# Optimization experiments

Hardware: AMD Instinct MI355X
Metric: run time of the kernel (lower is better)

Reference implementation:

```python
import jax, jax.numpy as jnp
import numpy as np


def setup_inputs() -> dict:
    key = jax.random.key(0)
    ks = jax.random.split(key, 6)
    B, N, D_in, D, Dg, H = 32, 256, 512, 256, 256, 512
    s = lambda f_in: 1.0 / np.sqrt(f_in)
    return {
        "xi": jax.random.normal(ks[0], (B, N, D_in), dtype=jnp.float32),
        "W_img": jax.random.normal(ks[1], (D_in, D), dtype=jnp.float32) * s(D_in),
        "b_img": jnp.zeros((D,), jnp.float32),
        "W_gnn_self": jax.random.normal(ks[2], (D, Dg), dtype=jnp.float32) * s(D),
        "W_gnn_nbr": jax.random.normal(ks[3], (D, Dg), dtype=jnp.float32) * s(D),
        "b_gnn": jnp.zeros((Dg,), jnp.float32),
        "W1": jax.random.normal(ks[4], (N * Dg, H), dtype=jnp.float32) * s(N * Dg),
        "b1": jnp.zeros((H,), jnp.float32),
        "W2": jax.random.normal(ks[5], (H, 1), dtype=jnp.float32) * s(H),
        "b2": jnp.zeros((1,), jnp.float32),
        "k": 10,
    }


def _knn_edges(xie, k):
    # xie: [B, N, D]. Per-image squared euclidean cdist + top-k (exclude self).
    B, N, _ = xie.shape
    x2 = jnp.sum(xie * xie, axis=-1)  # [B, N]
    d2 = x2[:, :, None] + x2[:, None, :] - 2.0 * jnp.einsum("bnd,bmd->bnm", xie, xie)
    big = jnp.asarray(1e30, d2.dtype)
    d2 = d2 + big * jnp.eye(N, dtype=d2.dtype)  # exclude self
    _, nbr = jax.lax.top_k(-d2, k)  # [B, N, k] neighbor (source) indices
    tgt = jnp.broadcast_to(jnp.arange(N)[None, :, None], (B, N, k))
    return nbr, tgt


def reference(xi, W_img, b_img, W_gnn_self, W_gnn_nbr, b_gnn, W1, b1, W2, b2, k):
    B, N, _ = xi.shape
    # image encoder -> per-node embeddings [B, N, D]
    xie = xi @ W_img + b_img
    # KNN graph build per image, then shift indices into one batched graph
    nbr, tgt = _knn_edges(xie, k)
    shift = (jnp.arange(B) * N)[:, None, None]
    src = (nbr + shift).reshape(-1)  # [B*N*k]
    dst = (tgt + shift).reshape(-1)  # [B*N*k]
    # batched graph conv: mean neighbor aggregation + self transform
    x_flat = xie.reshape(B * N, -1)
    agg = jax.ops.segment_sum(x_flat[src], dst, num_segments=B * N) / k
    gep = jax.nn.relu(x_flat @ W_gnn_self + agg @ W_gnn_nbr + b_gnn)
    gep = gep.reshape(B, N, -1)  # split_batch_graph
    # estimation MLP on flattened graph embedding
    h = jax.nn.relu(gep.reshape(B, -1) @ W1 + b1)
    out = h @ W2 + b2  # [B, 1]
    return xie, gep, out
```

## Files before the change

### kernel.cpp

```cpp
#include <hip/hip_runtime.h>

#define BB 32
#define NN 256
#define DIN 512
#define DD 256
#define HH 512
#define MM 8192
#define NDG 65536
#define KSTR 16

typedef __attribute__((ext_vector_type(8))) __bf16 bf16x8;
typedef __attribute__((ext_vector_type(4))) float f32x4;
typedef unsigned short ushort_t;

__device__ __forceinline__ unsigned short f2bf(float x) {
  unsigned u = __float_as_uint(x);
  u += 0x7FFFu + ((u >> 16) & 1u);
  return (unsigned short)(u >> 16);
}

__global__ __launch_bounds__(512) void k_enc(const float* __restrict__ A,
                                             const float* __restrict__ W,
                                             const float* __restrict__ bias,
                                             float* __restrict__ C,
                                             ushort_t* __restrict__ A_bf) {
  __shared__ float Asm[32][520];
  const int tid = threadIdx.x;
  const int mb0 = blockIdx.x * 32;
  const int cg = tid & 31;
  const int mh = (tid >> 5) & 7;
  const int team = tid >> 8;
#pragma unroll
  for (int i = 0; i < 8; ++i) {
    int idx = tid + i * 512;
    int m = idx >> 7;
    int kq = idx & 127;
    float4 v = *reinterpret_cast<const float4*>(&A[(size_t)(mb0 + m) * DIN + kq * 4]);
    *reinterpret_cast<float4*>(&Asm[m][kq * 4]) = v;
  }
  __syncthreads();
  float4 acc[4][2] = {};
  const int kt0 = team * 256;
  const float* wp = &W[(size_t)kt0 * DD + cg * 8];
  float4 wA[4][2], wB[4][2];
#pragma unroll
  for (int j = 0; j < 4; ++j) {
    wA[j][0] = *reinterpret_cast<const float4*>(&wp[(size_t)j * DD]);
    wA[j][1] = *reinterpret_cast<const float4*>(&wp[(size_t)j * DD + 4]);
  }
  for (int it = 0; it < 64; ++it) {
    if (it < 63) {
#pragma unroll
      for (int j = 0; j < 4; ++j) {
        wB[j][0] = *reinterpret_cast<const float4*>(&wp[(size_t)((it + 1) * 4 + j) * DD]);
        wB[j][1] = *reinterpret_cast<const float4*>(&wp[(size_t)((it + 1) * 4 + j) * DD + 4]);
      }
    }
    const int kk = kt0 + it * 4;
#pragma unroll
    for (int r = 0; r < 4; ++r) {
      float4 a = *reinterpret_cast<const float4*>(&Asm[mh * 4 + r][kk]);
#pragma unroll
      for (int h = 0; h < 2; ++h) {
        acc[r][h].x += a.x * wA[0][h].x; acc[r][h].y += a.x * wA[0][h].y;
        acc[r][h].z += a.x * wA[0][h].z; acc[r][h].w += a.x * wA[0][h].w;
        acc[r][h].x += a.y * wA[1][h].x; acc[r][h].y += a.y * wA[1][h].y;
        acc[r][h].z += a.y * wA[1][h].z; acc[r][h].w += a.y * wA[1][h].w;
        acc[r][h].x += a.z * wA[2][h].x; acc[r][h].y += a.z * wA[2][h].y;
        acc[r][h].z += a.z * wA[2][h].z; acc[r][h].w += a.z * wA[2][h].w;
        acc[r][h].x += a.w * wA[3][h].x; acc[r][h].y += a.w * wA[3][h].y;
        acc[r][h].z += a.w * wA[3][h].z; acc[r][h].w += a.w * wA[3][h].w;
      }
    }
#pragma unroll
    for (int j = 0; j < 4; ++j) {
      wA[j][0] = wB[j][0]; wA[j][1] = wB[j][1];
    }
  }
  __syncthreads();
  float* red = &Asm[0][0];
  if (team == 1) {
#pragma unroll
    for (int r = 0; r < 4; ++r) {
      *reinterpret_cast<float4*>(&red[(mh * 4 + r) * 256 + cg * 8]) = acc[r][0];
      *reinterpret_cast<float4*>(&red[(mh * 4 + r) * 256 + cg * 8 + 4]) = acc[r][1];
    }
  }
  __syncthreads();
  if (team == 0) {
    float4 bv0 = *reinterpret_cast<const float4*>(&bias[cg * 8]);
    float4 bv1 = *reinterpret_cast<const float4*>(&bias[cg * 8 + 4]);
#pragma unroll
    for (int r = 0; r < 4; ++r) {
      const int row = mb0 + mh * 4 + r;
      float4 o0 = *reinterpret_cast<float4*>(&red[(mh * 4 + r) * 256 + cg * 8]);
      float4 o1 = *reinterpret_cast<float4*>(&red[(mh * 4 + r) * 256 + cg * 8 + 4]);
      float4 s0, s1;
      s0.x = acc[r][0].x + o0.x + bv0.x; s0.y = acc[r][0].y + o0.y + bv0.y;
      s0.z = acc[r][0].z + o0.z + bv0.z; s0.w = acc[r][0].w + o0.w + bv0.w;
      s1.x = acc[r][1].x + o1.x + bv1.x; s1.y = acc[r][1].y + o1.y + bv1.y;
      s1.z = acc[r][1].z + o1.z + bv1.z; s1.w = acc[r][1].w + o1.w + bv1.w;
      *reinterpret_cast<float4*>(&C[(size_t)row * DD + cg * 8]) = s0;
      *reinterpret_cast<float4*>(&C[(size_t)row * DD + cg * 8 + 4]) = s1;
      ushort4 ob0, ob1;
      ob0.x = f2bf(s0.x); ob0.y = f2bf(s0.y); ob0.z = f2bf(s0.z); ob0.w = f2bf(s0.w);
      ob1.x = f2bf(s1.x); ob1.y = f2bf(s1.y); ob1.z = f2bf(s1.z); ob1.w = f2bf(s1.w);
      *reinterpret_cast<ushort4*>(&A_bf[(size_t)row * 512 + cg * 8]) = ob0;
      *reinterpret_cast<ushort4*>(&A_bf[(size_t)row * 512 + cg * 8 + 4]) = ob1;
    }
  }
}

__global__ __launch_bounds__(256) void k_norm(const float* __restrict__ X,
                                              float* __restrict__ x2) {
  const int tid = threadIdx.x;
  const int row = blockIdx.x * 4 + (tid >> 6);
  const int lane = tid & 63;
  float4 v = *reinterpret_cast<const float4*>(&X[(size_t)row * DD + lane * 4]);
  float s = v.x * v.x + v.y * v.y + v.z * v.z + v.w * v.w;
#pragma unroll
  for (int off = 1; off < 64; off <<= 1) s += __shfl_xor(s, off);
  if (lane == 0) x2[row] = s;
}

__global__ __launch_bounds__(256) void k_dist(const float* __restrict__ X,
                                              const float* __restrict__ x2,
                                              float* __restrict__ d2) {
  __shared__ float As[16][68];
  __shared__ float Bs[16][68];
  const int tid = threadIdx.x;
  const int b = blockIdx.z;
  const int m0 = blockIdx.x * 64, n0 = blockIdx.y * 64;
  const float* Xb = X + b * NN * DD;
  const int tx = tid & 15, ty = tid >> 4;
  const int lrow = tid >> 2, lfc = (tid & 3) * 4;
  float acc[4][4] = {};
  for (int k0 = 0; k0 < DD; k0 += 16) {
    float4 va = *reinterpret_cast<const float4*>(&Xb[(n0 + lrow) * DD + k0 + lfc]);
    As[lfc + 0][lrow] = va.x; As[lfc + 1][lrow] = va.y;
    As[lfc + 2][lrow] = va.z; As[lfc + 3][lrow] = va.w;
    float4 vb = *reinterpret_cast<const float4*>(&Xb[(m0 + lrow) * DD + k0 + lfc]);
    Bs[lfc + 0][lrow] = vb.x; Bs[lfc + 1][lrow] = vb.y;
    Bs[lfc + 2][lrow] = vb.z; Bs[lfc + 3][lrow] = vb.w;
    __syncthreads();
#pragma unroll
    for (int kk = 0; kk < 16; ++kk) {
      float a[4], bv[4];
      *reinterpret_cast<float4*>(a) = *reinterpret_cast<float4*>(&As[kk][ty * 4]);
      *reinterpret_cast<float4*>(bv) = *reinterpret_cast<float4*>(&Bs[kk][tx * 4]);
#pragma unroll
      for (int i = 0; i < 4; ++i)
#pragma unroll
        for (int j = 0; j < 4; ++j) acc[i][j] += a[i] * bv[j];
    }
    __syncthreads();
  }
#pragma unroll
  for (int i = 0; i < 4; ++i) {
    const int n = n0 + ty * 4 + i;
    const float xn = x2[b * NN + n];
    float4 v;
    float* vv = reinterpret_cast<float*>(&v);
#pragma unroll
    for (int j = 0; j < 4; ++j) {
      const int mc = m0 + tx * 4 + j;
      float dv = xn + x2[b * NN + mc] - 2.0f * acc[i][j];
      if (n == mc) dv = 1e30f;
      vv[j] = dv;
    }
    *reinterpret_cast<float4*>(&d2[(size_t)(b * NN + n) * NN + m0 + tx * 4]) = v;
  }
}

__global__ __launch_bounds__(256) void k_topk(const float* __restrict__ d2,
                                              const int* __restrict__ kp,
                                              int* __restrict__ nbr) {
  const int tid = threadIdx.x;
  const int i = blockIdx.x * 4 + (tid >> 6);
  const int lane = tid & 63;
  const int kcnt = kp[0];
  const float* row = d2 + (size_t)i * NN;
  float v0 = row[lane];
  float v1 = row[lane + 64];
  float v2 = row[lane + 128];
  float v3 = row[lane + 192];
  for (int it = 0; it < kcnt; ++it) {
    float v = v0; int idx = lane;
    if (v1 < v) { v = v1; idx = lane + 64; }
    if (v2 < v) { v = v2; idx = lane + 128; }
    if (v3 < v) { v = v3; idx = lane + 192; }
#pragma unroll
    for (int off = 1; off < 64; off <<= 1) {
      float ov = __shfl_xor(v, off);
      int oi = __shfl_xor(idx, off);
      if (ov < v || (ov == v && oi < idx)) { v = ov; idx = oi; }
    }
    if (lane == 0) nbr[i * KSTR + it] = idx;
    const int slot = idx >> 6;
    if (lane == (idx & 63)) {
      if (slot == 0) v0 = 3e38f;
      else if (slot == 1) v1 = 3e38f;
      else if (slot == 2) v2 = 3e38f;
      else v3 = 3e38f;
    }
  }
}

__global__ __launch_bounds__(256) void k_agg(const float* __restrict__ X,
                                             const int* __restrict__ nbr,
                                             const int* __restrict__ kp,
                                             ushort_t* __restrict__ A_bf) {
  const int i = blockIdx.x;
  const int b = i >> 8;
  const int t = threadIdx.x;
  const int kcnt = kp[0];
  float acc = 0.0f;
  for (int j = 0; j < kcnt; ++j) {
    const int nb = nbr[i * KSTR + j];
    acc += X[(size_t)(b * NN + nb) * DD + t];
  }
  A_bf[(size_t)i * 512 + 256 + t] = f2bf(acc / (float)kcnt);
}

__global__ __launch_bounds__(256) void k_cvtw(const float* __restrict__ Ws,
                                              const float* __restrict__ Wn,
                                              ushort_t* __restrict__ B_bfT) {
  const int id = blockIdx.x * 256 + threadIdx.x;
  const int k = id >> 8;
  const int n = id & 255;
  float v = (k < 256) ? Ws[(size_t)k * 256 + n] : Wn[(size_t)(k - 256) * 256 + n];
  B_bfT[(size_t)n * 512 + k] = f2bf(v);
}

__global__ __launch_bounds__(256) void k_gnn(const ushort_t* __restrict__ A_bf,
                                             const ushort_t* __restrict__ B_bfT,
                                             const float* __restrict__ bias,
                                             float* __restrict__ C,
                                             ushort_t* __restrict__ gep_bf) {
  __shared__ ushort_t As[64 * 72];
  __shared__ ushort_t Bs[64 * 72];
  const int tid = threadIdx.x;
  const int m0 = blockIdx.x * 64, n0 = blockIdx.y * 64;
  const int l = tid & 63, w = tid >> 6;
  const int mw = (w & 1) * 32, nw = (w >> 1) * 32;
  const int lr = tid >> 3, lq = tid & 7;
  f32x4 acc[2][2] = {};
  for (int kt = 0; kt < 8; ++kt) {
    const int kb = kt * 64;
#pragma unroll
    for (int s = 0; s < 2; ++s) {
      const int r = lr + s * 32;
      uint4 va = *reinterpret_cast<const uint4*>(&A_bf[(size_t)(m0 + r) * 512 + kb + lq * 8]);
      *reinterpret_cast<uint4*>(&As[r * 72 + lq * 8]) = va;
      uint4 vb = *reinterpret_cast<const uint4*>(&B_bfT[(size_t)(n0 + r) * 512 + kb + lq * 8]);
      *reinterpret_cast<uint4*>(&Bs[r * 72 + lq * 8]) = vb;
    }
    __syncthreads();
#pragma unroll
    for (int ks = 0; ks < 2; ++ks) {
      bf16x8 af[2], bf[2];
#pragma unroll
      for (int mi = 0; mi < 2; ++mi)
        af[mi] = *reinterpret_cast<const bf16x8*>(
            &As[(mw + mi * 16 + (l & 15)) * 72 + ks * 32 + (l >> 4) * 8]);
#pragma unroll
      for (int ni = 0; ni < 2; ++ni)
        bf[ni] = *reinterpret_cast<const bf16x8*>(
            &Bs[(nw + ni * 16 + (l & 15)) * 72 + ks * 32 + (l >> 4) * 8]);
#pragma unroll
      for (int mi = 0; mi < 2; ++mi)
#pragma unroll
        for (int ni = 0; ni < 2; ++ni)
          acc[mi][ni] = __builtin_amdgcn_mfma_f32_16x16x32_bf16(af[mi], bf[ni],
                                                                acc[mi][ni], 0, 0, 0);
    }
    __syncthreads();
  }
#pragma unroll
  for (int mi = 0; mi < 2; ++mi) {
    const int row_base = m0 + mw + mi * 16 + (l >> 4) * 4;
#pragma unroll
    for (int ni = 0; ni < 2; ++ni) {
      const int col = n0 + nw + ni * 16 + (l & 15);
      const float bv = bias[col];
#pragma unroll
      for (int r = 0; r < 4; ++r) {
        float v = acc[mi][ni][r] + bv;
        v = v > 0.0f ? v : 0.0f;
        C[(size_t)(row_base + r) * 256 + col] = v;
        gep_bf[(size_t)(row_base + r) * 256 + col] = f2bf(v);
      }
    }
  }
}

typedef const float __attribute__((address_space(1)))* gas1f;
typedef unsigned int __attribute__((address_space(3)))* las3u;

__global__ __launch_bounds__(256) void k_mlp1(const ushort_t* __restrict__ gep_bf,
                                              const float* __restrict__ W1,
                                              float* __restrict__ part) {
  __shared__ float Wb[2][32 * 512];
  __shared__ ushort_t Ab[32][264];
  const int tid = threadIdx.x;
  const int b = blockIdx.x;
  const int l = tid & 63, w = tid >> 6;
#pragma unroll
  for (int i = 0; i < 4; ++i) {
    int id = tid + i * 256;
    int m = id >> 5, dq8 = (id & 31) * 8;
    *reinterpret_cast<uint4*>(&Ab[m][dq8]) = *reinterpret_cast<const uint4*>(
        &gep_bf[((size_t)m * 256 + b) * 256 + dq8]);
  }
  const float* Wbase = W1 + (size_t)b * 256 * 512;
  auto stage = [&](int kt, int buf) {
    const float* gsrc = Wbase + (size_t)kt * 32 * 512;
#pragma unroll
    for (int i = 0; i < 16; ++i) {
      const int idx = w * 16 + i;
      const float* gp = gsrc + idx * 256 + l * 4;
      __builtin_amdgcn_global_load_lds((gas1f)gp, (las3u)&Wb[buf][idx * 256], 16, 0, 0);
    }
  };
  stage(0, 0);
  __syncthreads();
  const int n0w = w * 128;
  f32x4 acc[2][8] = {};
  for (int kt = 0; kt < 8; ++kt) {
    const int cur = kt & 1;
    if (kt < 7) stage(kt + 1, cur ^ 1);
    bf16x8 a[2];
#pragma unroll
    for (int mi = 0; mi < 2; ++mi)
      a[mi] = *reinterpret_cast<const bf16x8*>(&Ab[mi * 16 + (l & 15)][kt * 32 + (l >> 4) * 8]);
    const float* wl = &Wb[cur][0];
    const int kr = (l >> 4) * 8;
#pragma unroll
    for (int nf = 0; nf < 8; ++nf) {
      const int col = n0w + nf * 16 + (l & 15);
      union { unsigned short us[8]; bf16x8 v; } bb;
#pragma unroll
      for (int j = 0; j < 8; ++j)
        bb.us[j] = f2bf(wl[(kr + j) * 512 + col]);
      acc[0][nf] = __builtin_amdgcn_mfma_f32_16x16x32_bf16(a[0], bb.v, acc[0][nf], 0, 0, 0);
      acc[1][nf] = __builtin_amdgcn_mfma_f32_16x16x32_bf16(a[1], bb.v, acc[1][nf], 0, 0, 0);
    }
    __syncthreads();
  }
#pragma unroll
  for (int mi = 0; mi < 2; ++mi)
#pragma unroll
    for (int nf = 0; nf < 8; ++nf) {
      const int col = n0w + nf * 16 + (l & 15);
#pragma unroll
      for (int r = 0; r < 4; ++r) {
        const int m = mi * 16 + (l >> 4) * 4 + r;
        part[((size_t)b * 32 + m) * HH + col] = acc[mi][nf][r];
      }
    }
}

__global__ __launch_bounds__(256) void k_mlp1r(const float* __restrict__ part,
                                               const float* __restrict__ b1,
                                               float* __restrict__ h) {
  __shared__ float red[3][64];
  const int tid = threadIdx.x;
  const int m = blockIdx.x >> 3;
  const int c = (blockIdx.x & 7) * 64 + (tid & 63);
  const int bq = tid >> 6;
  float s = 0.0f;
  for (int bb = bq * 64; bb < bq * 64 + 64; ++bb)
    s += part[((size_t)bb * 32 + m) * 512 + c];
  if (bq > 0) red[bq - 1][tid & 63] = s;
  __syncthreads();
  if (bq == 0) {
    s += red[0][tid & 63] + red[1][tid & 63] + red[2][tid & 63];
    s += b1[c];
    h[m * HH + c] = s > 0.0f ? s : 0.0f;
  }
}

__global__ __launch_bounds__(256) void k_out(const float* __restrict__ h,
                                             const float* __restrict__ W2,
                                             const float* __restrict__ b2,
                                             float* __restrict__ outp) {
  const int tid = threadIdx.x;
  const int m = blockIdx.x * 4 + (tid >> 6);
  const int lane = tid & 63;
  float s = 0.0f;
#pragma unroll
  for (int j = 0; j < 8; ++j) s += h[m * HH + lane + 64 * j] * W2[lane + 64 * j];
#pragma unroll
  for (int off = 1; off < 64; off <<= 1) s += __shfl_xor(s, off);
  if (lane == 0) outp[m] = s + b2[0];
}

extern "C" void kernel_launch(void* const* d_in, const int* in_sizes, int n_in,
                              void* d_out, int out_size, void* d_ws, size_t ws_size,
                              hipStream_t stream) {
  const float* xi     = (const float*)d_in[0];
  const float* W_img  = (const float*)d_in[1];
  const float* b_img  = (const float*)d_in[2];
  const float* W_self = (const float*)d_in[3];
  const float* W_nbr  = (const float*)d_in[4];
  const float* b_gnn  = (const float*)d_in[5];
  const float* W1     = (const float*)d_in[6];
  const float* b1     = (const float*)d_in[7];
  const float* W2     = (const float*)d_in[8];
  const float* b2     = (const float*)d_in[9];
  const int*   kp     = (const int*)d_in[10];

  float* xie  = (float*)d_out;
  float* gep  = xie + (size_t)MM * DD;
  float* outp = gep + (size_t)MM * DD;

  float* ws   = (float*)d_ws;
  float* x2   = ws;
  int*   nbr  = (int*)(ws + 8192);
  float* d2   = ws + 8192 + 131072;
  float* part = d2 + (size_t)2097152;
  float* hbuf = part + (size_t)4194304;
  ushort_t* A_bf   = (ushort_t*)(hbuf + 16384);
  ushort_t* B_bfT  = A_bf + (size_t)MM * 512;
  ushort_t* gep_bf = B_bfT + 131072;

  k_enc  <<<MM / 32, 512, 0, stream>>>(xi, W_img, b_img, xie, A_bf);
  k_cvtw <<<512, 256, 0, stream>>>(W_self, W_nbr, B_bfT);
  k_norm <<<MM / 4, 256, 0, stream>>>(xie, x2);
  k_dist <<<dim3(4, 4, BB), 256, 0, stream>>>(xie, x2, d2);
  k_topk <<<MM / 4, 256, 0, stream>>>(d2, kp, nbr);
  k_agg  <<<MM, 256, 0, stream>>>(xie, nbr, kp, A_bf);
  k_gnn  <<<dim3(128, 4), 256, 0, stream>>>(A_bf, B_bfT, b_gnn, gep, gep_bf);
  k_mlp1 <<<256, 256, 0, stream>>>(gep_bf, W1, part);
  k_mlp1r<<<256, 256, 0, stream>>>(part, b1, hbuf);
  k_out  <<<8, 256, 0, stream>>>(hbuf, W2, b2, outp);
}
```

Measured before the change: 160.0 us.

## Fuse distance, top-k and aggregation into one kernel; merge MLP tail kernels

The encoder now also writes a transposed copy of the embeddings, so the new fused kernel can compute each 32-row distance block against the whole image. Top-k selection and neighbor mean aggregation then run in the same kernel, which removes the d2 and nbr round trips through global memory and two launches. The final reduction, ReLU and output dot product are merged into a single kernel. In exchange there are fewer blocks (256) for the distance work, an extra transposed write in the encoder, and the final kernel's 32 blocks each read the full partial buffer serially.

Result: slower. 230.6 us (+44.1%).

```diff
diff --git a/kernel.cpp b/kernel.cpp
--- a/kernel.cpp
+++ b/kernel.cpp
@@ -6,7 +6,6 @@
 #define DD 256
 #define HH 512
 #define MM 8192
-#define NDG 65536
 #define KSTR 16
 
 typedef __attribute__((ext_vector_type(8))) __bf16 bf16x8;
@@ -23,7 +22,8 @@
                                              const float* __restrict__ W,
                                              const float* __restrict__ bias,
                                              float* __restrict__ C,
-                                             ushort_t* __restrict__ A_bf) {
+                                             ushort_t* __restrict__ A_bf,
+                                             float* __restrict__ xieT) {
   __shared__ float Asm[32][520];
   const int tid = threadIdx.x;
   const int mb0 = blockIdx.x * 32;
@@ -107,7 +107,23 @@
       ob1.x = f2bf(s1.x); ob1.y = f2bf(s1.y); ob1.z = f2bf(s1.z); ob1.w = f2bf(s1.w);
       *reinterpret_cast<ushort4*>(&A_bf[(size_t)row * 512 + cg * 8]) = ob0;
       *reinterpret_cast<ushort4*>(&A_bf[(size_t)row * 512 + cg * 8 + 4]) = ob1;
-    }
+      *reinterpret_cast<float4*>(&red[(mh * 4 + r) * 256 + cg * 8]) = s0;
+      *reinterpret_cast<float4*>(&red[(mh * 4 + r) * 256 + cg * 8 + 4]) = s1;
+    }
+  }
+  __syncthreads();
+  {
+    const int b = mb0 >> 8;
+    const int n0b = mb0 & 255;
+    const int d = tid >> 1;
+    const int nh = (tid & 1) * 16;
+    float tmp[16];
+#pragma unroll
+    for (int i = 0; i < 16; ++i) tmp[i] = red[(nh + i) * 256 + d];
+    float* dst = &xieT[((size_t)b * 256 + d) * 256 + n0b + nh];
+#pragma unroll
+    for (int i = 0; i < 4; ++i)
+      *reinterpret_cast<float4*>(&dst[i * 4]) = *reinterpret_cast<float4*>(&tmp[i * 4]);
   }
 }
 
@@ -123,103 +139,112 @@
   if (lane == 0) x2[row] = s;
 }
 
-__global__ __launch_bounds__(256) void k_dist(const float* __restrict__ X,
-                                              const float* __restrict__ x2,
-                                              float* __restrict__ d2) {
-  __shared__ float As[16][68];
-  __shared__ float Bs[16][68];
-  const int tid = threadIdx.x;
-  const int b = blockIdx.z;
-  const int m0 = blockIdx.x * 64, n0 = blockIdx.y * 64;
-  const float* Xb = X + b * NN * DD;
-  const int tx = tid & 15, ty = tid >> 4;
-  const int lrow = tid >> 2, lfc = (tid & 3) * 4;
-  float acc[4][4] = {};
-  for (int k0 = 0; k0 < DD; k0 += 16) {
-    float4 va = *reinterpret_cast<const float4*>(&Xb[(n0 + lrow) * DD + k0 + lfc]);
-    As[lfc + 0][lrow] = va.x; As[lfc + 1][lrow] = va.y;
-    As[lfc + 2][lrow] = va.z; As[lfc + 3][lrow] = va.w;
-    float4 vb = *reinterpret_cast<const float4*>(&Xb[(m0 + lrow) * DD + k0 + lfc]);
-    Bs[lfc + 0][lrow] = vb.x; Bs[lfc + 1][lrow] = vb.y;
-    Bs[lfc + 2][lrow] = vb.z; Bs[lfc + 3][lrow] = vb.w;
-    __syncthreads();
-#pragma unroll
-    for (int kk = 0; kk < 16; ++kk) {
-      float a[4], bv[4];
-      *reinterpret_cast<float4*>(a) = *reinterpret_cast<float4*>(&As[kk][ty * 4]);
-      *reinterpret_cast<float4*>(bv) = *reinterpret_cast<float4*>(&Bs[kk][tx * 4]);
-#pragma unroll
-      for (int i = 0; i < 4; ++i)
-#pragma unroll
-        for (int j = 0; j < 4; ++j) acc[i][j] += a[i] * bv[j];
-    }
-    __syncthreads();
-  }
+__global__ __launch_bounds__(512) void k_dist(const float* __restrict__ xie,
+                                              const float* __restrict__ xieT,
+                                              const float* __restrict__ x2g,
+                                              const int* __restrict__ kp,
+                                              ushort_t* __restrict__ A_bf) {
+  __shared__ float Asm[32][260];
+  __shared__ int nbrL[32][KSTR];
+  const int tid = threadIdx.x;
+  const int b = blockIdx.x >> 3;
+  const int n0b = (blockIdx.x & 7) * 32;
+  const int base = b * 256;
+  const int r = tid >> 4;
+  const int c = tid & 15;
+  const int kcnt = kp[0];
 #pragma unroll
   for (int i = 0; i < 4; ++i) {
-    const int n = n0 + ty * 4 + i;
-    const float xn = x2[b * NN + n];
-    float4 v;
-    float* vv = reinterpret_cast<float*>(&v);
-#pragma unroll
-    for (int j = 0; j < 4; ++j) {
-      const int mc = m0 + tx * 4 + j;
-      float dv = xn + x2[b * NN + mc] - 2.0f * acc[i][j];
-      if (n == mc) dv = 1e30f;
-      vv[j] = dv;
-    }
-    *reinterpret_cast<float4*>(&d2[(size_t)(b * NN + n) * NN + m0 + tx * 4]) = v;
-  }
-}
-
-__global__ __launch_bounds__(256) void k_topk(const float* __restrict__ d2,
-                                              const int* __restrict__ kp,
-                                              int* __restrict__ nbr) {
-  const int tid = threadIdx.x;
-  const int i = blockIdx.x * 4 + (tid >> 6);
-  const int lane = tid & 63;
-  const int kcnt = kp[0];
-  const float* row = d2 + (size_t)i * NN;
-  float v0 = row[lane];
-  float v1 = row[lane + 64];
-  float v2 = row[lane + 128];
-  float v3 = row[lane + 192];
-  for (int it = 0; it < kcnt; ++it) {
-    float v = v0; int idx = lane;
-    if (v1 < v) { v = v1; idx = lane + 64; }
-    if (v2 < v) { v = v2; idx = lane + 128; }
-    if (v3 < v) { v = v3; idx = lane + 192; }
-#pragma unroll
-    for (int off = 1; off < 64; off <<= 1) {
-      float ov = __shfl_xor(v, off);
-      int oi = __shfl_xor(idx, off);
-      if (ov < v || (ov == v && oi < idx)) { v = ov; idx = oi; }
-    }
-    if (lane == 0) nbr[i * KSTR + it] = idx;
-    const int slot = idx >> 6;
-    if (lane == (idx & 63)) {
-      if (slot == 0) v0 = 3e38f;
-      else if (slot == 1) v1 = 3e38f;
-      else if (slot == 2) v2 = 3e38f;
-      else v3 = 3e38f;
-    }
-  }
-}
-
-__global__ __launch_bounds__(256) void k_agg(const float* __restrict__ X,
-                                             const int* __restrict__ nbr,
-                                             const int* __restrict__ kp,
-                                             ushort_t* __restrict__ A_bf) {
-  const int i = blockIdx.x;
-  const int b = i >> 8;
-  const int t = threadIdx.x;
-  const int kcnt = kp[0];
-  float acc = 0.0f;
-  for (int j = 0; j < kcnt; ++j) {
-    const int nb = nbr[i * KSTR + j];
-    acc += X[(size_t)(b * NN + nb) * DD + t];
-  }
-  A_bf[(size_t)i * 512 + 256 + t] = f2bf(acc / (float)kcnt);
+    int idx = tid + i * 512;
+    int m = idx >> 6;
+    int kq = idx & 63;
+    float4 v = *reinterpret_cast<const float4*>(
+        &xie[(size_t)(base + n0b + m) * DD + kq * 4]);
+    *reinterpret_cast<float4*>(&Asm[m][kq * 4]) = v;
+  }
+  __syncthreads();
+  float4 acc4[4] = {};
+  const float* wp = &xieT[(size_t)base * 256 + c * 16];
+  for (int it = 0; it < 64; ++it) {
+    float4 a = *reinterpret_cast<const float4*>(&Asm[r][it * 4]);
+#pragma unroll
+    for (int dj = 0; dj < 4; ++dj) {
+      const float* row = wp + (size_t)(it * 4 + dj) * 256;
+      float4 w0 = *reinterpret_cast<const float4*>(&row[0]);
+      float4 w1 = *reinterpret_cast<const float4*>(&row[4]);
+      float4 w2 = *reinterpret_cast<const float4*>(&row[8]);
+      float4 w3 = *reinterpret_cast<const float4*>(&row[12]);
+      const float ad = (dj == 0) ? a.x : (dj == 1) ? a.y : (dj == 2) ? a.z : a.w;
+      acc4[0].x += ad * w0.x; acc4[0].y += ad * w0.y;
+      acc4[0].z += ad * w0.z; acc4[0].w += ad * w0.w;
+      acc4[1].x += ad * w1.x; acc4[1].y += ad * w1.y;
+      acc4[1].z += ad * w1.z; acc4[1].w += ad * w1.w;
+      acc4[2].x += ad * w2.x; acc4[2].y += ad * w2.y;
+      acc4[2].z += ad * w2.z; acc4[2].w += ad * w2.w;
+      acc4[3].x += ad * w3.x; acc4[3].y += ad * w3.y;
+      acc4[3].z += ad * w3.z; acc4[3].w += ad * w3.w;
+    }
+  }
+  const int nl = n0b + r;
+  const float xn = x2g[base + nl];
+  float v[16];
+#pragma unroll
+  for (int q = 0; q < 4; ++q) {
+    const float* accp = reinterpret_cast<const float*>(&acc4[q]);
+#pragma unroll
+    for (int j2 = 0; j2 < 4; ++j2) {
+      const int mc = c * 16 + q * 4 + j2;
+      float dv = xn + x2g[base + mc] - 2.0f * accp[j2];
+      if (nl == mc) dv = 1e30f;
+      v[q * 4 + j2] = dv;
+    }
+  }
+  for (int it2 = 0; it2 < kcnt; ++it2) {
+    float lv = v[0]; int li = 0;
+#pragma unroll
+    for (int j = 1; j < 16; ++j)
+      if (v[j] < lv) { lv = v[j]; li = j; }
+    int midx = c * 16 + li;
+#pragma unroll
+    for (int off = 1; off < 16; off <<= 1) {
+      float ov = __shfl_xor(lv, off);
+      int oi = __shfl_xor(midx, off);
+      if (ov < lv || (ov == lv && oi < midx)) { lv = ov; midx = oi; }
+    }
+    if (c == 0) nbrL[r][it2] = midx;
+    const bool mine = (c == (midx >> 4));
+    const int jw = midx & 15;
+#pragma unroll
+    for (int j = 0; j < 16; ++j)
+      v[j] = (mine && j == jw) ? 3e38f : v[j];
+  }
+  __syncthreads();
+  {
+    const int row = tid >> 4;
+    const int q0 = (tid & 15) * 16;
+    float4 a4[4] = {};
+    for (int j = 0; j < kcnt; ++j) {
+      const int nb = nbrL[row][j];
+      const float* src = &xie[(size_t)(base + nb) * DD + q0];
+#pragma unroll
+      for (int q = 0; q < 4; ++q) {
+        float4 vv = *reinterpret_cast<const float4*>(&src[q * 4]);
+        a4[q].x += vv.x; a4[q].y += vv.y; a4[q].z += vv.z; a4[q].w += vv.w;
+      }
+    }
+    const float sc = 1.0f / (float)kcnt;
+    ushort_t ob[16];
+#pragma unroll
+    for (int q = 0; q < 4; ++q) {
+      ob[q * 4 + 0] = f2bf(a4[q].x * sc);
+      ob[q * 4 + 1] = f2bf(a4[q].y * sc);
+      ob[q * 4 + 2] = f2bf(a4[q].z * sc);
+      ob[q * 4 + 3] = f2bf(a4[q].w * sc);
+    }
+    ushort_t* dst = &A_bf[(size_t)(base + n0b + row) * 512 + 256 + q0];
+    *reinterpret_cast<uint4*>(&dst[0]) = *reinterpret_cast<uint4*>(&ob[0]);
+    *reinterpret_cast<uint4*>(&dst[8]) = *reinterpret_cast<uint4*>(&ob[8]);
+  }
 }
 
 __global__ __launch_bounds__(256) void k_cvtw(const float* __restrict__ Ws,
@@ -360,39 +385,32 @@
     }
 }
 
-__global__ __launch_bounds__(256) void k_mlp1r(const float* __restrict__ part,
-                                               const float* __restrict__ b1,
-                                               float* __restrict__ h) {
-  __shared__ float red[3][64];
-  const int tid = threadIdx.x;
-  const int m = blockIdx.x >> 3;
-  const int c = (blockIdx.x & 7) * 64 + (tid & 63);
-  const int bq = tid >> 6;
-  float s = 0.0f;
-  for (int bb = bq * 64; bb < bq * 64 + 64; ++bb)
-    s += part[((size_t)bb * 32 + m) * 512 + c];
-  if (bq > 0) red[bq - 1][tid & 63] = s;
-  __syncthreads();
-  if (bq == 0) {
-    s += red[0][tid & 63] + red[1][tid & 63] + red[2][tid & 63];
-    s += b1[c];
-    h[m * HH + c] = s > 0.0f ? s : 0.0f;
-  }
-}
-
-__global__ __launch_bounds__(256) void k_out(const float* __restrict__ h,
+__global__ __launch_bounds__(256) void k_fin(const float* __restrict__ part,
+                                             const float* __restrict__ b1,
                                              const float* __restrict__ W2,
                                              const float* __restrict__ b2,
                                              float* __restrict__ outp) {
-  const int tid = threadIdx.x;
-  const int m = blockIdx.x * 4 + (tid >> 6);
-  const int lane = tid & 63;
-  float s = 0.0f;
-#pragma unroll
-  for (int j = 0; j < 8; ++j) s += h[m * HH + lane + 64 * j] * W2[lane + 64 * j];
-#pragma unroll
-  for (int off = 1; off < 64; off <<= 1) s += __shfl_xor(s, off);
-  if (lane == 0) outp[m] = s + b2[0];
+  __shared__ float red[4];
+  const int tid = threadIdx.x;
+  const int m = blockIdx.x;
+  const int c0 = tid * 2;
+  float s0 = 0.f, s1 = 0.f, s2 = 0.f, s3 = 0.f;
+  for (int bb = 0; bb < 256; bb += 2) {
+    float2 v0 = *reinterpret_cast<const float2*>(&part[((size_t)bb * 32 + m) * 512 + c0]);
+    float2 v1 = *reinterpret_cast<const float2*>(&part[((size_t)(bb + 1) * 32 + m) * 512 + c0]);
+    s0 += v0.x; s1 += v0.y; s2 += v1.x; s3 += v1.y;
+  }
+  float h0 = s0 + s2 + b1[c0];
+  float h1 = s1 + s3 + b1[c0 + 1];
+  h0 = h0 > 0.f ? h0 : 0.f;
+  h1 = h1 > 0.f ? h1 : 0.f;
+  float val = h0 * W2[c0] + h1 * W2[c0 + 1];
+#pragma unroll
+  for (int off = 1; off < 64; off <<= 1) val += __shfl_xor(val, off);
+  const int w = tid >> 6;
+  if ((tid & 63) == 0) red[w] = val;
+  __syncthreads();
+  if (tid == 0) outp[m] = red[0] + red[1] + red[2] + red[3] + b2[0];
 }
 
 extern "C" void kernel_launch(void* const* d_in, const int* in_sizes, int n_in,
@@ -416,22 +434,17 @@
 
   float* ws   = (float*)d_ws;
   float* x2   = ws;
-  int*   nbr  = (int*)(ws + 8192);
-  float* d2   = ws + 8192 + 131072;
-  float* part = d2 + (size_t)2097152;
-  float* hbuf = part + (size_t)4194304;
-  ushort_t* A_bf   = (ushort_t*)(hbuf + 16384);
+  float* part = ws + 8192;
+  float* xieT = part + 4194304;
+  ushort_t* A_bf   = (ushort_t*)(xieT + 2097152);
   ushort_t* B_bfT  = A_bf + (size_t)MM * 512;
   ushort_t* gep_bf = B_bfT + 131072;
 
-  k_enc  <<<MM / 32, 512, 0, stream>>>(xi, W_img, b_img, xie, A_bf);
+  k_enc  <<<MM / 32, 512, 0, stream>>>(xi, W_img, b_img, xie, A_bf, xieT);
   k_cvtw <<<512, 256, 0, stream>>>(W_self, W_nbr, B_bfT);
   k_norm <<<MM / 4, 256, 0, stream>>>(xie, x2);
-  k_dist <<<dim3(4, 4, BB), 256, 0, stream>>>(xie, x2, d2);
-  k_topk <<<MM / 4, 256, 0, stream>>>(d2, kp, nbr);
-  k_agg  <<<MM, 256, 0, stream>>>(xie, nbr, kp, A_bf);
+  k_dist <<<256, 512, 0, stream>>>(xie, xieT, x2, kp, A_bf);
   k_gnn  <<<dim3(128, 4), 256, 0, stream>>>(A_bf, B_bfT, b_gnn, gep, gep_bf);
   k_mlp1 <<<256, 256, 0, stream>>>(gep_bf, W1, part);
-  k_mlp1r<<<256, 256, 0, stream>>>(part, b1, hbuf);
-  k_out  <<<8, 256, 0, stream>>>(hbuf, W2, b2, outp);
-}
+  k_fin  <<<BB, 256, 0, stream>>>(part, b1, W2, b2, outp);
+}
```

## Stage W1 as transposed bf16 in LDS via registers and fuse MLP tail kernels

Applied to the files above, without the earlier changes.

The MLP1 kernel now loads W1 into registers, converts it to bf16 once, and stores it transposed in LDS so each MFMA B-fragment is a single vector LDS read. Previously every wave re-converted eight strided fp32 LDS values per fragment. The block is widened to 512 threads with fewer output tiles per wave. The partial-sum reduction, bias+ReLU and the final W2 dot product are merged into one kernel, removing a launch and the intermediate h buffer, though the merged kernel runs only 32 blocks.

Measured after the change: 152.6 us. -4.6%, faster.

```diff
diff --git a/kernel.cpp b/kernel.cpp
--- a/kernel.cpp
+++ b/kernel.cpp
@@ -6,7 +6,6 @@
 #define DD 256
 #define HH 512
 #define MM 8192
-#define NDG 65536
 #define KSTR 16
 
 typedef __attribute__((ext_vector_type(8))) __bf16 bf16x8;
@@ -294,63 +293,70 @@
   }
 }
 
-typedef const float __attribute__((address_space(1)))* gas1f;
-typedef unsigned int __attribute__((address_space(3)))* las3u;
-
-__global__ __launch_bounds__(256) void k_mlp1(const ushort_t* __restrict__ gep_bf,
+__global__ __launch_bounds__(512) void k_mlp1(const ushort_t* __restrict__ gep_bf,
                                               const float* __restrict__ W1,
                                               float* __restrict__ part) {
-  __shared__ float Wb[2][32 * 512];
+  __shared__ ushort_t WbT[2][512][40];
   __shared__ ushort_t Ab[32][264];
   const int tid = threadIdx.x;
   const int b = blockIdx.x;
   const int l = tid & 63, w = tid >> 6;
 #pragma unroll
-  for (int i = 0; i < 4; ++i) {
-    int id = tid + i * 256;
+  for (int i = 0; i < 2; ++i) {
+    int id = tid + i * 512;
     int m = id >> 5, dq8 = (id & 31) * 8;
     *reinterpret_cast<uint4*>(&Ab[m][dq8]) = *reinterpret_cast<const uint4*>(
         &gep_bf[((size_t)m * 256 + b) * 256 + dq8]);
   }
-  const float* Wbase = W1 + (size_t)b * 256 * 512;
-  auto stage = [&](int kt, int buf) {
-    const float* gsrc = Wbase + (size_t)kt * 32 * 512;
-#pragma unroll
-    for (int i = 0; i < 16; ++i) {
-      const int idx = w * 16 + i;
-      const float* gp = gsrc + idx * 256 + l * 4;
-      __builtin_amdgcn_global_load_lds((gas1f)gp, (las3u)&Wb[buf][idx * 256], 16, 0, 0);
-    }
+  const float* Wbase = W1 + (size_t)b * 256 * 512 + tid;
+  float wreg[32];
+  auto WLOAD = [&](int s) {
+#pragma unroll
+    for (int kk = 0; kk < 32; ++kk)
+      wreg[kk] = Wbase[(size_t)(s * 32 + kk) * 512];
   };
-  stage(0, 0);
+  auto WSTORE = [&](int buf) {
+#pragma unroll
+    for (int q = 0; q < 4; ++q) {
+      ushort_t tmp[8];
+#pragma unroll
+      for (int j = 0; j < 8; ++j) tmp[j] = f2bf(wreg[q * 8 + j]);
+      *reinterpret_cast<uint4*>(&WbT[buf][tid][q * 8]) =
+          *reinterpret_cast<const uint4*>(tmp);
+    }
+  };
+  WLOAD(0);
+  WSTORE(0);
   __syncthreads();
-  const int n0w = w * 128;
-  f32x4 acc[2][8] = {};
-  for (int kt = 0; kt < 8; ++kt) {
-    const int cur = kt & 1;
-    if (kt < 7) stage(kt + 1, cur ^ 1);
-    bf16x8 a[2];
+  const int n0w = w * 64;
+  f32x4 acc[2][4] = {};
+  for (int s = 0; s < 8; ++s) {
+    const int cur = s & 1;
+    if (s < 7) WLOAD(s + 1);
+    bf16x8 a[2], bw[4];
 #pragma unroll
     for (int mi = 0; mi < 2; ++mi)
-      a[mi] = *reinterpret_cast<const bf16x8*>(&Ab[mi * 16 + (l & 15)][kt * 32 + (l >> 4) * 8]);
-    const float* wl = &Wb[cur][0];
-    const int kr = (l >> 4) * 8;
-#pragma unroll
-    for (int nf = 0; nf < 8; ++nf) {
-      const int col = n0w + nf * 16 + (l & 15);
-      union { unsigned short us[8]; bf16x8 v; } bb;
-#pragma unroll
-      for (int j = 0; j < 8; ++j)
-        bb.us[j] = f2bf(wl[(kr + j) * 512 + col]);
-      acc[0][nf] = __builtin_amdgcn_mfma_f32_16x16x32_bf16(a[0], bb.v, acc[0][nf], 0, 0, 0);
-      acc[1][nf] = __builtin_amdgcn_mfma_f32_16x16x32_bf16(a[1], bb.v, acc[1][nf], 0, 0, 0);
-    }
-    __syncthreads();
+      a[mi] = *reinterpret_cast<const bf16x8*>(
+          &Ab[mi * 16 + (l & 15)][s * 32 + (l >> 4) * 8]);
+#pragma unroll
+    for (int nf = 0; nf < 4; ++nf)
+      bw[nf] = *reinterpret_cast<const bf16x8*>(
+          &WbT[cur][n0w + nf * 16 + (l & 15)][(l >> 4) * 8]);
+#pragma unroll
+    for (int mi = 0; mi < 2; ++mi)
+#pragma unroll
+      for (int nf = 0; nf < 4; ++nf)
+        acc[mi][nf] = __builtin_amdgcn_mfma_f32_16x16x32_bf16(a[mi], bw[nf],
+                                                              acc[mi][nf], 0, 0, 0);
+    if (s < 7) {
+      WSTORE(cur ^ 1);
+      __syncthreads();
+    }
   }
 #pragma unroll
   for (int mi = 0; mi < 2; ++mi)
 #pragma unroll
-    for (int nf = 0; nf < 8; ++nf) {
+    for (int nf = 0; nf < 4; ++nf) {
       const int col = n0w + nf * 16 + (l & 15);
 #pragma unroll
       for (int r = 0; r < 4; ++r) {
@@ -360,39 +366,32 @@
     }
 }
 
-__global__ __launch_bounds__(256) void k_mlp1r(const float* __restrict__ part,
-                                               const float* __restrict__ b1,
-                                               float* __restrict__ h) {
-  __shared__ float red[3][64];
-  const int tid = threadIdx.x;
-  const int m = blockIdx.x >> 3;
-  const int c = (blockIdx.x & 7) * 64 + (tid & 63);
-  const int bq = tid >> 6;
-  float s = 0.0f;
-  for (int bb = bq * 64; bb < bq * 64 + 64; ++bb)
-    s += part[((size_t)bb * 32 + m) * 512 + c];
-  if (bq > 0) red[bq - 1][tid & 63] = s;
-  __syncthreads();
-  if (bq == 0) {
-    s += red[0][tid & 63] + red[1][tid & 63] + red[2][tid & 63];
-    s += b1[c];
-    h[m * HH + c] = s > 0.0f ? s : 0.0f;
-  }
-}
-
-__global__ __launch_bounds__(256) void k_out(const float* __restrict__ h,
+__global__ __launch_bounds__(256) void k_fin(const float* __restrict__ part,
+                                             const float* __restrict__ b1,
                                              const float* __restrict__ W2,
                                              const float* __restrict__ b2,
                                              float* __restrict__ outp) {
-  const int tid = threadIdx.x;
-  const int m = blockIdx.x * 4 + (tid >> 6);
-  const int lane = tid & 63;
-  float s = 0.0f;
-#pragma unroll
-  for (int j = 0; j < 8; ++j) s += h[m * HH + lane + 64 * j] * W2[lane + 64 * j];
-#pragma unroll
-  for (int off = 1; off < 64; off <<= 1) s += __shfl_xor(s, off);
-  if (lane == 0) outp[m] = s + b2[0];
+  __shared__ float red[4];
+  const int tid = threadIdx.x;
+  const int m = blockIdx.x;
+  const int c0 = tid * 2;
+  float s0 = 0.f, s1 = 0.f, s2 = 0.f, s3 = 0.f;
+  for (int bb = 0; bb < 256; bb += 2) {
+    float2 v0 = *reinterpret_cast<const float2*>(&part[((size_t)bb * 32 + m) * 512 + c0]);
+    float2 v1 = *reinterpret_cast<const float2*>(&part[((size_t)(bb + 1) * 32 + m) * 512 + c0]);
+    s0 += v0.x; s1 += v0.y; s2 += v1.x; s3 += v1.y;
+  }
+  float h0 = s0 + s2 + b1[c0];
+  float h1 = s1 + s3 + b1[c0 + 1];
+  h0 = h0 > 0.f ? h0 : 0.f;
+  h1 = h1 > 0.f ? h1 : 0.f;
+  float val = h0 * W2[c0] + h1 * W2[c0 + 1];
+#pragma unroll
+  for (int off = 1; off < 64; off <<= 1) val += __shfl_xor(val, off);
+  const int w = tid >> 6;
+  if ((tid & 63) == 0) red[w] = val;
+  __syncthreads();
+  if (tid == 0) outp[m] = red[0] + red[1] + red[2] + red[3] + b2[0];
 }
 
 extern "C" void kernel_launch(void* const* d_in, const int* in_sizes, int n_in,
@@ -419,8 +418,7 @@
   int*   nbr  = (int*)(ws + 8192);
   float* d2   = ws + 8192 + 131072;
   float* part = d2 + (size_t)2097152;
-  float* hbuf = part + (size_t)4194304;
-  ushort_t* A_bf   = (ushort_t*)(hbuf + 16384);
+  ushort_t* A_bf   = (ushort_t*)(part + 4194304);
   ushort_t* B_bfT  = A_bf + (size_t)MM * 512;
   ushort_t* gep_bf = B_bfT + 131072;
 
@@ -431,7 +429,6 @@
   k_topk <<<MM / 4, 256, 0, stream>>>(d2, kp, nbr);
   k_agg  <<<MM, 256, 0, stream>>>(xie, nbr, kp, A_bf);
   k_gnn  <<<dim3(128, 4), 256, 0, stream>>>(A_bf, B_bfT, b_gnn, gep, gep_bf);
-  k_mlp1 <<<256, 256, 0, stream>>>(gep_bf, W1, part);
-  k_mlp1r<<<256, 256, 0, stream>>>(part, b1, hbuf);
-  k_out  <<<8, 256, 0, stream>>>(hbuf, W2, b2, outp);
-}
+  k_mlp1 <<<256, 512, 0, stream>>>(gep_bf, W1, part);
+  k_fin  <<<BB, 256, 0, stream>>>(part, b1, W2, b2, outp);
+}
```
